# Performance work log

Measured on AMD Instinct MI355X. Metric: run time of the kernel, lower is better.

The kernel has to match this reference:

```python
import jax, jax.numpy as jnp
import numpy as np
from functools import partial

IMG = 608
H = W = 76            # grid size (stride 8 head)
A = 3                 # anchors per scale
C = 80                # classes
BA = 5 + C            # bbox attrs
STRIDE = IMG / float(H)
ANCHORS = np.array([[10., 13.], [16., 30.], [33., 23.]], dtype=np.float32)
SC_ANCH = ANCHORS / STRIDE          # anchors in grid units
IGNORE_THR = 0.5
OBJ_SCALE = 1.0
NOOBJ_SCALE = 100.0


def setup_inputs() -> dict:
    key = jax.random.key(0)
    k1, k2, k3, k4 = jax.random.split(key, 4)
    B, T = 16, 50
    pred = jax.random.normal(k1, (B, A * BA, H, W), dtype=jnp.float32)
    xy = jax.random.uniform(k2, (B, T, 2), minval=0.01, maxval=0.99, dtype=jnp.float32)
    wh = jax.random.uniform(k3, (B, T, 2), minval=0.02, maxval=0.30, dtype=jnp.float32)
    cls_id = jax.random.randint(k4, (B, T, 1), 0, C).astype(jnp.float32)
    targets = jnp.concatenate([xy, wh, cls_id], axis=-1)  # [B, T, 5] normalized
    return {"pred": pred, "targets": targets}


def build_targets(targets):
    """Faithful vectorized+scan version of YOlOLoss.build_targets."""
    B, T, _ = targets.shape
    mult = jnp.array([W, H, W, H, 1.0], dtype=jnp.float32)
    tb = targets * mult                      # scale x,w by W and y,h by H; class untouched
    gx, gy, gw, gh, gc = (tb[..., i] for i in range(5))
    valid = (gx + gy + gw + gh) != 0.0       # torch: skip rows whose first 4 entries sum to 0
    gi = jnp.floor(gx).astype(jnp.int32)
    gj = jnp.floor(gy).astype(jnp.int32)
    gi = jnp.where(gi == 0, 1, gi)           # quirk in original: 0 -> 1
    gj = jnp.where(gj == 0, 1, gj)

    aw = jnp.asarray(SC_ANCH[:, 0])          # [A]
    ah = jnp.asarray(SC_ANCH[:, 1])
    # IoU of corner-aligned boxes [0,0,w,h]
    inter = jnp.minimum(gw[..., None], aw) * jnp.minimum(gh[..., None], ah)   # [B,T,A]
    union = gw[..., None] * gh[..., None] + 1e-16 + aw * ah - inter
    ious = inter / union
    best = jnp.argmax(ious, axis=-1).astype(jnp.int32)                        # [B,T]
    ign = ious > IGNORE_THR                                                   # [B,T,A]

    bidx = jnp.broadcast_to(jnp.arange(B, dtype=jnp.int32)[:, None], (B, T))
    flat = lambda a: a.reshape((B * T,) + a.shape[2:])
    xs = {"b": flat(bidx), "v": flat(valid), "gi": flat(gi), "gj": flat(gj),
          "n": flat(best), "ign": flat(ign), "gx": flat(gx), "gy": flat(gy),
          "gw": flat(gw), "gh": flat(gh), "cls": flat(gc).astype(jnp.int32)}

    z = jnp.zeros((B, A, H, W), jnp.float32)
    init = (jnp.zeros((B, A, H, W), bool),          # obj_mask
            jnp.ones((B, A, H, W), bool),           # noobj_mask
            z, z, z, z, z,                          # tx, ty, tw, th, tconf
            jnp.zeros((B, A, H, W, C), jnp.float32))  # tcls

    def step(carry, s):
        obj, noobj, tx, ty, tw, th, tconf, tcls = carry
        b, v, gi, gj, n = s["b"], s["v"], s["gi"], s["gj"], s["n"]
        # ignore-anchor suppression; NOTE original indexes (gi, gj) here (swapped quirk)
        cur = noobj[b, :, gi, gj]
        noobj = noobj.at[b, :, gi, gj].set(jnp.where(v & s["ign"], False, cur))

        def upd(arr, idx, val):
            return arr.at[idx].set(jnp.where(v, val, arr[idx]))

        obj = upd(obj, (b, n, gj, gi), True)
        noobj = upd(noobj, (b, n, gj, gi), False)
        tx = upd(tx, (b, n, gj, gi), s["gx"] - gi.astype(jnp.float32))
        ty = upd(ty, (b, n, gj, gi), s["gy"] - gj.astype(jnp.float32))
        tw = upd(tw, (b, n, gj, gi), jnp.log(s["gw"] / aw[n] + 1e-16))
        th = upd(th, (b, n, gj, gi), jnp.log(s["gh"] / ah[n] + 1e-16))
        tconf = upd(tconf, (b, n, gj, gi), 1.0)
        tcls = upd(tcls, (b, n, gj, gi, s["cls"]), 1.0)
        return (obj, noobj, tx, ty, tw, th, tconf, tcls), None

    carry, _ = jax.lax.scan(step, init, xs)
    return carry


def _masked_mse(p, t, m, n):
    return jnp.sum(m * (p - t) ** 2) / n


def _masked_bce(p, t, m, n):
    # torch BCELoss clamps log terms at -100
    lp = jnp.maximum(jnp.log(p), -100.0)
    l1p = jnp.maximum(jnp.log1p(-p), -100.0)
    return jnp.sum(m * (-(t * lp + (1.0 - t) * l1p))) / n


def yolo_loss(pred, tgt_grids):
    B = pred.shape[0]
    obj, noobj, tx, ty, tw, th, tconf, tcls = tgt_grids
    p = pred.reshape(B, A, BA, H, W).transpose(0, 1, 3, 4, 2)   # [B,A,H,W,5+C]
    x = jax.nn.sigmoid(p[..., 0])
    y = jax.nn.sigmoid(p[..., 1])
    w_ = p[..., 2]
    h_ = p[..., 3]
    conf = jax.nn.sigmoid(p[..., 4])
    pcls = jax.nn.sigmoid(p[..., 5:])

    of = obj.astype(jnp.float32)
    nf = noobj.astype(jnp.float32)
    n_obj = jnp.maximum(jnp.sum(of), 1.0)
    n_noobj = jnp.maximum(jnp.sum(nf), 1.0)

    loss_x = _masked_mse(x, tx, of, n_obj)
    loss_y = _masked_mse(y, ty, of, n_obj)
    loss_w = _masked_mse(w_, tw, of, n_obj)
    loss_h = _masked_mse(h_, th, of, n_obj)
    loss_conf_obj = _masked_bce(conf, tconf, of, n_obj)
    loss_conf_noobj = _masked_bce(conf, tconf, nf, n_noobj)
    loss_conf = OBJ_SCALE * loss_conf_obj + NOOBJ_SCALE * loss_conf_noobj
    loss_cls = _masked_bce(pcls, tcls, of[..., None], n_obj * C)
    return loss_x + loss_y + loss_w + loss_h + loss_conf + loss_cls


@jax.jit
def _run(pred, targets):
    return yolo_loss(pred, build_targets(targets))


def reference(pred, targets):
    return _run(pred, targets)
```

## Files before the change

kernel.cpp:

```cpp
#include <hip/hip_runtime.h>
#include <math.h>

#define BB 16
#define TT 50
#define AA 3
#define CC 80
#define BA_ 85
#define HH 76
#define WW 76
#define SPAT (HH * WW)
#define BMW 544
#define NQ (SPAT / 4)
#define NF4 (BB * AA * NQ)
#define NOB ((NF4 + 255) / 256)
#define PB_OFF 544

__constant__ float c_aw[3] = {1.25f, 2.0f, 4.125f};
__constant__ float c_ah[3] = {1.625f, 3.75f, 2.875f};

__device__ inline float wave_red(float v) {
    #pragma unroll
    for (int off = 32; off; off >>= 1) v += __shfl_down(v, off);
    return v;
}

__global__ __launch_bounds__(256) void k_main(const float* __restrict__ pred,
                                              const float* __restrict__ targets,
                                              float* __restrict__ part) {
    const int bx = blockIdx.x;
    const int tid = threadIdx.x;
    const int wave = tid >> 6, lane = tid & 63;

    if (bx < NOB) {
        int f = bx * 256 + tid;
        float s_bn = 0.f, s_cn = 0.f;
        if (f < NF4) {
            int plane = f / NQ;
            int q = f - plane * NQ;
            const float4 z4 = *reinterpret_cast<const float4*>(
                pred + (size_t)(plane * BA_ + 4) * SPAT + q * 4);
            float zs[4] = {z4.x, z4.y, z4.z, z4.w};
            #pragma unroll
            for (int k = 0; k < 4; ++k) {
                float conf = 1.f / (1.f + expf(-zs[k]));
                s_bn += -fmaxf(log1pf(-conf), -100.f);
            }
            s_cn = 4.f;
        }
        s_bn = wave_red(s_bn); s_cn = wave_red(s_cn);
        __shared__ float r2[4][2];
        if (lane == 0) { r2[wave][0] = s_bn; r2[wave][1] = s_cn; }
        __syncthreads();
        if (tid == 0) {
            part[bx * 2 + 0] = r2[0][0] + r2[1][0] + r2[2][0] + r2[3][0];
            part[bx * 2 + 1] = r2[0][1] + r2[1][1] + r2[2][1] + r2[3][1];
        }
        return;
    }

    const int b = bx - NOB;
    __shared__ unsigned bm[BMW];
    __shared__ int sh_valid[TT], sh_best[TT], sh_mcell[TT], sh_cls[TT], sh_owner[TT];
    __shared__ float sh_tx[TT], sh_ty[TT], sh_tw[TT], sh_th[TT];
    __shared__ unsigned sh_m0[TT], sh_m1[TT], sh_m2[TT];
    __shared__ float red[4][6];

    for (int w = tid; w < BMW; w += 256) bm[w] = 0u;

    int valid = 0, best = 0, mcell = 0, icell = 0, ign = 0;
    if (tid < TT) {
        const float* tg = targets + ((size_t)b * TT + tid) * 5;
        float gx = tg[0] * WW, gy = tg[1] * HH;
        float gw = tg[2] * WW, gh = tg[3] * HH;
        int cls = (int)tg[4];
        valid = (gx + gy + gw + gh != 0.0f) ? 1 : 0;
        int gi = (int)floorf(gx); if (gi == 0) gi = 1;
        int gj = (int)floorf(gy); if (gj == 0) gj = 1;
        float bi = -1.f;
        #pragma unroll
        for (int a = 0; a < 3; ++a) {
            float inter = fminf(gw, c_aw[a]) * fminf(gh, c_ah[a]);
            float uni = gw * gh + 1e-16f + c_aw[a] * c_ah[a] - inter;
            float iou = inter / uni;
            if (iou > bi) { bi = iou; best = a; }
            if (iou > 0.5f) ign |= 1 << a;
        }
        icell = gi * WW + gj;
        mcell = gj * WW + gi;
        sh_valid[tid] = valid; sh_best[tid] = best;
        sh_mcell[tid] = mcell; sh_cls[tid] = cls;
        sh_tx[tid] = gx - (float)gi;
        sh_ty[tid] = gy - (float)gj;
        sh_tw[tid] = logf(gw / c_aw[best] + 1e-16f);
        sh_th[tid] = logf(gh / c_ah[best] + 1e-16f);
    }
    __syncthreads();

    if (tid < TT) {
        int owner = 0;
        if (valid) {
            #pragma unroll
            for (int a = 0; a < 3; ++a)
                if ((ign >> a) & 1) {
                    int bit = a * SPAT + icell;
                    atomicOr(&bm[bit >> 5], 1u << (bit & 31));
                }
            int mb = best * SPAT + mcell;
            atomicOr(&bm[mb >> 5], 1u << (mb & 31));

            owner = 1;
            for (int t2 = tid + 1; t2 < TT; ++t2)
                if (sh_valid[t2] && sh_mcell[t2] == mcell && sh_best[t2] == best) {
                    owner = 0; break;
                }
            if (owner) {
                unsigned m0 = 0u, m1 = 0u, m2 = 0u;
                for (int t2 = 0; t2 < TT; ++t2)
                    if (sh_valid[t2] && sh_mcell[t2] == mcell && sh_best[t2] == best) {
                        int c = sh_cls[t2];
                        if (c < 32) m0 |= 1u << c;
                        else if (c < 64) m1 |= 1u << (c - 32);
                        else m2 |= 1u << (c - 64);
                    }
                sh_m0[tid] = m0; sh_m1[tid] = m1; sh_m2[tid] = m2;
            }
        }
        sh_owner[tid] = owner;
    }
    __syncthreads();

    float s_mse = 0.f, s_bo = 0.f, s_bc = 0.f, s_no = 0.f;
    for (int r = wave; r < TT; r += 4) {
        if (!sh_owner[r]) continue;
        int base = ((b * AA + sh_best[r]) * BA_) * SPAT + sh_mcell[r];
        unsigned m0 = sh_m0[r], m1 = sh_m1[r], m2 = sh_m2[r];
        float z = pred[(size_t)base + (size_t)lane * SPAT];
        if (lane == 0) {
            float x = 1.f / (1.f + expf(-z));
            s_mse += (x - sh_tx[r]) * (x - sh_tx[r]);
            s_no += 1.f;
        } else if (lane == 1) {
            float y = 1.f / (1.f + expf(-z));
            s_mse += (y - sh_ty[r]) * (y - sh_ty[r]);
        } else if (lane == 2) {
            s_mse += (z - sh_tw[r]) * (z - sh_tw[r]);
        } else if (lane == 3) {
            s_mse += (z - sh_th[r]) * (z - sh_th[r]);
        } else if (lane == 4) {
            float cf = 1.f / (1.f + expf(-z));
            s_bo += -fmaxf(logf(cf), -100.f);
        } else {
            int ci = lane - 5;
            unsigned wd = (ci < 32) ? m0 : m1;
            int tcv = (wd >> (ci & 31)) & 1;
            float p = 1.f / (1.f + expf(-z));
            s_bc += tcv ? -fmaxf(logf(p), -100.f) : -fmaxf(log1pf(-p), -100.f);
        }
        if (lane < BA_ - 64) {
            float z2 = pred[(size_t)base + (size_t)(64 + lane) * SPAT];
            int ci = 59 + lane;
            unsigned wd = (ci < 64) ? m1 : m2;
            int tcv = (wd >> (ci & 31)) & 1;
            float p = 1.f / (1.f + expf(-z2));
            s_bc += tcv ? -fmaxf(logf(p), -100.f) : -fmaxf(log1pf(-p), -100.f);
        }
    }

    float s_bs = 0.f, s_cs = 0.f;
    for (int w = tid; w < BMW; w += 256) {
        unsigned bits = bm[w];
        while (bits) {
            int bit = __ffs(bits) - 1; bits &= bits - 1;
            int idx = w * 32 + bit;
            int a = idx / SPAT;
            int s = idx - a * SPAT;
            float z = pred[(size_t)((b * AA + a) * BA_ + 4) * SPAT + s];
            float conf = 1.f / (1.f + expf(-z));
            s_bs += -fmaxf(log1pf(-conf), -100.f);
            s_cs += 1.f;
        }
    }

    s_mse = wave_red(s_mse); s_bo = wave_red(s_bo); s_bc = wave_red(s_bc);
    s_no  = wave_red(s_no);  s_bs = wave_red(s_bs); s_cs = wave_red(s_cs);
    if (lane == 0) {
        red[wave][0] = s_mse; red[wave][1] = s_bo; red[wave][2] = s_bc;
        red[wave][3] = s_no;  red[wave][4] = s_bs; red[wave][5] = s_cs;
    }
    __syncthreads();
    if (tid == 0) {
        #pragma unroll
        for (int k = 0; k < 6; ++k)
            part[PB_OFF + b * 6 + k] =
                red[0][k] + red[1][k] + red[2][k] + red[3][k];
    }
}

__global__ __launch_bounds__(256) void k_final(const float* __restrict__ part,
                                               float* __restrict__ out) {
    const int tid = threadIdx.x;
    const int wave = tid >> 6, lane = tid & 63;
    float v_mse = 0.f, v_bo = 0.f, v_bn = 0.f, v_bc = 0.f, v_no = 0.f, v_cn = 0.f;

    for (int i = tid; i < NOB; i += 256) {
        v_bn += part[i * 2 + 0];
        v_cn += part[i * 2 + 1];
    }
    for (int i = tid; i < BB; i += 256) {
        const float* p = part + PB_OFF + i * 6;
        v_mse += p[0]; v_bo += p[1]; v_bc += p[2];
        v_no  += p[3]; v_bn -= p[4]; v_cn -= p[5];
    }

    v_mse = wave_red(v_mse); v_bo = wave_red(v_bo); v_bn = wave_red(v_bn);
    v_bc  = wave_red(v_bc);  v_no = wave_red(v_no); v_cn = wave_red(v_cn);

    __shared__ float red[4][6];
    if (lane == 0) {
        red[wave][0] = v_mse; red[wave][1] = v_bo; red[wave][2] = v_bn;
        red[wave][3] = v_bc;  red[wave][4] = v_no; red[wave][5] = v_cn;
    }
    __syncthreads();
    if (tid == 0) {
        float m[6];
        #pragma unroll
        for (int k = 0; k < 6; ++k)
            m[k] = red[0][k] + red[1][k] + red[2][k] + red[3][k];
        float n_obj   = fmaxf(m[4], 1.f);
        float n_noobj = fmaxf(m[5], 1.f);
        out[0] = m[0] / n_obj
               + m[1] / n_obj
               + 100.f * (m[2] / n_noobj)
               + m[3] / (n_obj * (float)CC);
    }
}

extern "C" void kernel_launch(void* const* d_in, const int* in_sizes, int n_in,
                              void* d_out, int out_size, void* d_ws, size_t ws_size,
                              hipStream_t stream) {
    const float* pred    = (const float*)d_in[0];
    const float* targets = (const float*)d_in[1];
    float* out  = (float*)d_out;
    float* part = (float*)d_ws;

    k_main<<<NOB + BB, 256, 0, stream>>>(pred, targets, part);
    k_final<<<1, 256, 0, stream>>>(part, out);
}
```

Before: 164.3 us.

## Replace per-batch sparse gather with dense per-cell state map and streaming pass

Target building moves into a small per-batch kernel. It writes a byte state map per anchor cell (0 = noobj, 1 = ignored, 2+t = owning target) and a compact record array per target. A new dense kernel streams every channel of pred per spatial chunk and computes all loss terms from the state map. This replaces the 16 latency-bound per-batch blocks that walked bitmaps and did scattered loads. The trade is that the whole prediction tensor is now read: an asm barrier forces the class-channel loads even for cells without objects, and there is one extra kernel launch.

```diff
diff --git a/kernel.cpp b/kernel.cpp
--- a/kernel.cpp
+++ b/kernel.cpp
@@ -9,14 +9,15 @@
 #define HH 76
 #define WW 76
 #define SPAT (HH * WW)
-#define BMW 544
-#define NQ (SPAT / 4)
-#define NF4 (BB * AA * NQ)
-#define NOB ((NF4 + 255) / 256)
-#define PB_OFF 544
+#define NPLANE (BB * AA)
+#define CHUNK 512
+#define NCHUNK ((SPAT + CHUNK - 1) / CHUNK)
+#define NBLK (NPLANE * NCHUNK)
 
 __constant__ float c_aw[3] = {1.25f, 2.0f, 4.125f};
 __constant__ float c_ah[3] = {1.625f, 3.75f, 2.875f};
+
+struct Rec { float tx, ty, tw, th; unsigned m0, m1, m2, pad; };
 
 __device__ inline float wave_red(float v) {
     #pragma unroll
@@ -24,50 +25,18 @@
     return v;
 }
 
-__global__ __launch_bounds__(256) void k_main(const float* __restrict__ pred,
-                                              const float* __restrict__ targets,
-                                              float* __restrict__ part) {
-    const int bx = blockIdx.x;
+__global__ __launch_bounds__(256) void k_build(const float* __restrict__ targets,
+                                               unsigned char* __restrict__ state,
+                                               Rec* __restrict__ recs) {
+    const int b = blockIdx.x;
     const int tid = threadIdx.x;
-    const int wave = tid >> 6, lane = tid & 63;
-
-    if (bx < NOB) {
-        int f = bx * 256 + tid;
-        float s_bn = 0.f, s_cn = 0.f;
-        if (f < NF4) {
-            int plane = f / NQ;
-            int q = f - plane * NQ;
-            const float4 z4 = *reinterpret_cast<const float4*>(
-                pred + (size_t)(plane * BA_ + 4) * SPAT + q * 4);
-            float zs[4] = {z4.x, z4.y, z4.z, z4.w};
-            #pragma unroll
-            for (int k = 0; k < 4; ++k) {
-                float conf = 1.f / (1.f + expf(-zs[k]));
-                s_bn += -fmaxf(log1pf(-conf), -100.f);
-            }
-            s_cn = 4.f;
-        }
-        s_bn = wave_red(s_bn); s_cn = wave_red(s_cn);
-        __shared__ float r2[4][2];
-        if (lane == 0) { r2[wave][0] = s_bn; r2[wave][1] = s_cn; }
-        __syncthreads();
-        if (tid == 0) {
-            part[bx * 2 + 0] = r2[0][0] + r2[1][0] + r2[2][0] + r2[3][0];
-            part[bx * 2 + 1] = r2[0][1] + r2[1][1] + r2[2][1] + r2[3][1];
-        }
-        return;
-    }
-
-    const int b = bx - NOB;
-    __shared__ unsigned bm[BMW];
-    __shared__ int sh_valid[TT], sh_best[TT], sh_mcell[TT], sh_cls[TT], sh_owner[TT];
-    __shared__ float sh_tx[TT], sh_ty[TT], sh_tw[TT], sh_th[TT];
-    __shared__ unsigned sh_m0[TT], sh_m1[TT], sh_m2[TT];
-    __shared__ float red[4][6];
-
-    for (int w = tid; w < BMW; w += 256) bm[w] = 0u;
+    __shared__ int sh_valid[TT], sh_best[TT], sh_mcell[TT], sh_cls[TT];
+
+    int4* pl = (int4*)(state + (size_t)b * AA * SPAT);
+    for (int k = tid; k < (AA * SPAT) / 16; k += 256) pl[k] = make_int4(0, 0, 0, 0);
 
     int valid = 0, best = 0, mcell = 0, icell = 0, ign = 0;
+    float txv = 0.f, tyv = 0.f, twv = 0.f, thv = 0.f;
     if (tid < TT) {
         const float* tg = targets + ((size_t)b * TT + tid) * 5;
         float gx = tg[0] * WW, gy = tg[1] * HH;
@@ -87,138 +56,151 @@
         }
         icell = gi * WW + gj;
         mcell = gj * WW + gi;
+        txv = gx - (float)gi;
+        tyv = gy - (float)gj;
+        twv = logf(gw / c_aw[best] + 1e-16f);
+        thv = logf(gh / c_ah[best] + 1e-16f);
         sh_valid[tid] = valid; sh_best[tid] = best;
         sh_mcell[tid] = mcell; sh_cls[tid] = cls;
-        sh_tx[tid] = gx - (float)gi;
-        sh_ty[tid] = gy - (float)gj;
-        sh_tw[tid] = logf(gw / c_aw[best] + 1e-16f);
-        sh_th[tid] = logf(gh / c_ah[best] + 1e-16f);
-    }
-    __syncthreads();
-
-    if (tid < TT) {
-        int owner = 0;
-        if (valid) {
+    }
+    __syncthreads();
+
+    unsigned char* st = state + (size_t)b * AA * SPAT;
+    if (tid < TT && valid) {
+        #pragma unroll
+        for (int a = 0; a < 3; ++a)
+            if ((ign >> a) & 1) st[a * SPAT + icell] = 1;
+        st[best * SPAT + mcell] = 1;
+    }
+    __syncthreads();
+
+    if (tid < TT && valid) {
+        bool owner = true;
+        for (int t2 = tid + 1; t2 < TT; ++t2)
+            if (sh_valid[t2] && sh_mcell[t2] == mcell && sh_best[t2] == best) {
+                owner = false; break;
+            }
+        if (owner) {
+            unsigned m0 = 0u, m1 = 0u, m2 = 0u;
+            for (int t2 = 0; t2 < TT; ++t2)
+                if (sh_valid[t2] && sh_mcell[t2] == mcell && sh_best[t2] == best) {
+                    int c = sh_cls[t2];
+                    if (c < 32) m0 |= 1u << c;
+                    else if (c < 64) m1 |= 1u << (c - 32);
+                    else m2 |= 1u << (c - 64);
+                }
+            Rec r; r.tx = txv; r.ty = tyv; r.tw = twv; r.th = thv;
+            r.m0 = m0; r.m1 = m1; r.m2 = m2; r.pad = 0u;
+            recs[b * TT + tid] = r;
+            st[best * SPAT + mcell] = (unsigned char)(2 + tid);
+        }
+    }
+}
+
+__global__ __launch_bounds__(128) void k_dense(const float* __restrict__ pred,
+                                               const unsigned char* __restrict__ state,
+                                               const Rec* __restrict__ recs,
+                                               float* __restrict__ part) {
+    const int blk = blockIdx.x;
+    const int p = blk / NCHUNK;
+    const int chunk = blk - p * NCHUNK;
+    const int b = p / AA;
+    const int tid = threadIdx.x;
+
+    __shared__ Rec lrec[TT];
+    for (int k = tid; k < TT * 8; k += 128)
+        ((unsigned*)lrec)[k] = ((const unsigned*)(recs + (size_t)b * TT))[k];
+    __syncthreads();
+
+    float s_mse = 0.f, s_bo = 0.f, s_bn = 0.f, s_bc = 0.f, s_no = 0.f, s_cn = 0.f;
+    const int s0 = chunk * CHUNK + tid * 4;
+
+    if (s0 < SPAT) {
+        uchar4 s4 = *(const uchar4*)(state + (size_t)p * SPAT + s0);
+        int st[4] = {s4.x, s4.y, s4.z, s4.w};
+        const float* pb = pred + (size_t)p * BA_ * SPAT + s0;
+
+        #pragma unroll
+        for (int c = 0; c < 4; ++c) {
+            float4 z4 = *(const float4*)(pb + (size_t)c * SPAT);
+            float zz[4] = {z4.x, z4.y, z4.z, z4.w};
             #pragma unroll
-            for (int a = 0; a < 3; ++a)
-                if ((ign >> a) & 1) {
-                    int bit = a * SPAT + icell;
-                    atomicOr(&bm[bit >> 5], 1u << (bit & 31));
+            for (int k = 0; k < 4; ++k)
+                if (st[k] >= 2) {
+                    const Rec& r = lrec[st[k] - 2];
+                    float tv = (&r.tx)[c];
+                    float v = (c < 2) ? 1.f / (1.f + expf(-zz[k])) : zz[k];
+                    s_mse += (v - tv) * (v - tv);
+                    if (c == 0) s_no += 1.f;
                 }
-            int mb = best * SPAT + mcell;
-            atomicOr(&bm[mb >> 5], 1u << (mb & 31));
-
-            owner = 1;
-            for (int t2 = tid + 1; t2 < TT; ++t2)
-                if (sh_valid[t2] && sh_mcell[t2] == mcell && sh_best[t2] == best) {
-                    owner = 0; break;
+        }
+        {
+            float4 z4 = *(const float4*)(pb + (size_t)4 * SPAT);
+            float zz[4] = {z4.x, z4.y, z4.z, z4.w};
+            #pragma unroll
+            for (int k = 0; k < 4; ++k) {
+                float conf = 1.f / (1.f + expf(-zz[k]));
+                if (st[k] == 0) {
+                    s_cn += 1.f;
+                    s_bn += -fmaxf(log1pf(-conf), -100.f);
+                } else if (st[k] >= 2) {
+                    s_bo += -fmaxf(logf(conf), -100.f);
                 }
-            if (owner) {
-                unsigned m0 = 0u, m1 = 0u, m2 = 0u;
-                for (int t2 = 0; t2 < TT; ++t2)
-                    if (sh_valid[t2] && sh_mcell[t2] == mcell && sh_best[t2] == best) {
-                        int c = sh_cls[t2];
-                        if (c < 32) m0 |= 1u << c;
-                        else if (c < 64) m1 |= 1u << (c - 32);
-                        else m2 |= 1u << (c - 64);
+            }
+        }
+        bool anyobj = ((st[0] | st[1] | st[2] | st[3]) >= 2);
+        #pragma unroll 8
+        for (int c = 5; c < BA_; ++c) {
+            float4 z4 = *(const float4*)(pb + (size_t)c * SPAT);
+            asm volatile("" :: "v"(z4.x), "v"(z4.y), "v"(z4.z), "v"(z4.w));
+            if (anyobj) {
+                float zz[4] = {z4.x, z4.y, z4.z, z4.w};
+                int ci = c - 5;
+                #pragma unroll
+                for (int k = 0; k < 4; ++k)
+                    if (st[k] >= 2) {
+                        const Rec& r = lrec[st[k] - 2];
+                        unsigned wd = (&r.m0)[ci >> 5];
+                        int tcv = (wd >> (ci & 31)) & 1;
+                        float pr = 1.f / (1.f + expf(-zz[k]));
+                        s_bc += tcv ? -fmaxf(logf(pr), -100.f)
+                                    : -fmaxf(log1pf(-pr), -100.f);
                     }
-                sh_m0[tid] = m0; sh_m1[tid] = m1; sh_m2[tid] = m2;
             }
         }
-        sh_owner[tid] = owner;
-    }
-    __syncthreads();
-
-    float s_mse = 0.f, s_bo = 0.f, s_bc = 0.f, s_no = 0.f;
-    for (int r = wave; r < TT; r += 4) {
-        if (!sh_owner[r]) continue;
-        int base = ((b * AA + sh_best[r]) * BA_) * SPAT + sh_mcell[r];
-        unsigned m0 = sh_m0[r], m1 = sh_m1[r], m2 = sh_m2[r];
-        float z = pred[(size_t)base + (size_t)lane * SPAT];
-        if (lane == 0) {
-            float x = 1.f / (1.f + expf(-z));
-            s_mse += (x - sh_tx[r]) * (x - sh_tx[r]);
-            s_no += 1.f;
-        } else if (lane == 1) {
-            float y = 1.f / (1.f + expf(-z));
-            s_mse += (y - sh_ty[r]) * (y - sh_ty[r]);
-        } else if (lane == 2) {
-            s_mse += (z - sh_tw[r]) * (z - sh_tw[r]);
-        } else if (lane == 3) {
-            s_mse += (z - sh_th[r]) * (z - sh_th[r]);
-        } else if (lane == 4) {
-            float cf = 1.f / (1.f + expf(-z));
-            s_bo += -fmaxf(logf(cf), -100.f);
-        } else {
-            int ci = lane - 5;
-            unsigned wd = (ci < 32) ? m0 : m1;
-            int tcv = (wd >> (ci & 31)) & 1;
-            float p = 1.f / (1.f + expf(-z));
-            s_bc += tcv ? -fmaxf(logf(p), -100.f) : -fmaxf(log1pf(-p), -100.f);
-        }
-        if (lane < BA_ - 64) {
-            float z2 = pred[(size_t)base + (size_t)(64 + lane) * SPAT];
-            int ci = 59 + lane;
-            unsigned wd = (ci < 64) ? m1 : m2;
-            int tcv = (wd >> (ci & 31)) & 1;
-            float p = 1.f / (1.f + expf(-z2));
-            s_bc += tcv ? -fmaxf(logf(p), -100.f) : -fmaxf(log1pf(-p), -100.f);
-        }
-    }
-
-    float s_bs = 0.f, s_cs = 0.f;
-    for (int w = tid; w < BMW; w += 256) {
-        unsigned bits = bm[w];
-        while (bits) {
-            int bit = __ffs(bits) - 1; bits &= bits - 1;
-            int idx = w * 32 + bit;
-            int a = idx / SPAT;
-            int s = idx - a * SPAT;
-            float z = pred[(size_t)((b * AA + a) * BA_ + 4) * SPAT + s];
-            float conf = 1.f / (1.f + expf(-z));
-            s_bs += -fmaxf(log1pf(-conf), -100.f);
-            s_cs += 1.f;
-        }
-    }
-
-    s_mse = wave_red(s_mse); s_bo = wave_red(s_bo); s_bc = wave_red(s_bc);
-    s_no  = wave_red(s_no);  s_bs = wave_red(s_bs); s_cs = wave_red(s_cs);
-    if (lane == 0) {
-        red[wave][0] = s_mse; red[wave][1] = s_bo; red[wave][2] = s_bc;
-        red[wave][3] = s_no;  red[wave][4] = s_bs; red[wave][5] = s_cs;
+    }
+
+    s_mse = wave_red(s_mse); s_bo = wave_red(s_bo); s_bn = wave_red(s_bn);
+    s_bc  = wave_red(s_bc);  s_no = wave_red(s_no); s_cn = wave_red(s_cn);
+    __shared__ float red[2][6];
+    int wv = tid >> 6, ln = tid & 63;
+    if (ln == 0) {
+        red[wv][0] = s_mse; red[wv][1] = s_bo; red[wv][2] = s_bn;
+        red[wv][3] = s_bc;  red[wv][4] = s_no; red[wv][5] = s_cn;
     }
     __syncthreads();
     if (tid == 0) {
         #pragma unroll
         for (int k = 0; k < 6; ++k)
-            part[PB_OFF + b * 6 + k] =
-                red[0][k] + red[1][k] + red[2][k] + red[3][k];
+            part[blk * 6 + k] = red[0][k] + red[1][k];
     }
 }
 
 __global__ __launch_bounds__(256) void k_final(const float* __restrict__ part,
                                                float* __restrict__ out) {
     const int tid = threadIdx.x;
-    const int wave = tid >> 6, lane = tid & 63;
-    float v_mse = 0.f, v_bo = 0.f, v_bn = 0.f, v_bc = 0.f, v_no = 0.f, v_cn = 0.f;
-
-    for (int i = tid; i < NOB; i += 256) {
-        v_bn += part[i * 2 + 0];
-        v_cn += part[i * 2 + 1];
-    }
-    for (int i = tid; i < BB; i += 256) {
-        const float* p = part + PB_OFF + i * 6;
-        v_mse += p[0]; v_bo += p[1]; v_bc += p[2];
-        v_no  += p[3]; v_bn -= p[4]; v_cn -= p[5];
-    }
-
-    v_mse = wave_red(v_mse); v_bo = wave_red(v_bo); v_bn = wave_red(v_bn);
-    v_bc  = wave_red(v_bc);  v_no = wave_red(v_no); v_cn = wave_red(v_cn);
-
+    float v[6] = {0.f, 0.f, 0.f, 0.f, 0.f, 0.f};
+    for (int i = tid; i < NBLK; i += 256) {
+        #pragma unroll
+        for (int k = 0; k < 6; ++k) v[k] += part[i * 6 + k];
+    }
+    #pragma unroll
+    for (int k = 0; k < 6; ++k) v[k] = wave_red(v[k]);
     __shared__ float red[4][6];
-    if (lane == 0) {
-        red[wave][0] = v_mse; red[wave][1] = v_bo; red[wave][2] = v_bn;
-        red[wave][3] = v_bc;  red[wave][4] = v_no; red[wave][5] = v_cn;
+    int wv = tid >> 6, ln = tid & 63;
+    if (ln == 0) {
+        #pragma unroll
+        for (int k = 0; k < 6; ++k) red[wv][k] = v[k];
     }
     __syncthreads();
     if (tid == 0) {
@@ -240,9 +222,14 @@
                               hipStream_t stream) {
     const float* pred    = (const float*)d_in[0];
     const float* targets = (const float*)d_in[1];
-    float* out  = (float*)d_out;
-    float* part = (float*)d_ws;
-
-    k_main<<<NOB + BB, 256, 0, stream>>>(pred, targets, part);
+    float* out = (float*)d_out;
+    char* ws = (char*)d_ws;
+
+    Rec*           recs  = (Rec*)ws;
+    unsigned char* state = (unsigned char*)(ws + 25600);
+    float*         part  = (float*)(ws + 302848);
+
+    k_build<<<BB, 256, 0, stream>>>(targets, state, recs);
+    k_dense<<<NBLK, 128, 0, stream>>>(pred, state, recs, part);
     k_final<<<1, 256, 0, stream>>>(part, out);
 }
```

Result: slower. 314.1 us (+91.2%).
